# Kernel tuning notes

Measured on AMD Instinct MI355X. Metric: run time of the kernel, lower is better.

The kernel has to match this reference:

```python
import jax, jax.numpy as jnp
import numpy as np

EMB = 1024
H = 16
D = EMB // H  # 64
EPS = 1e-5
SM_SCALE = 1.0  # forward default sm_scale=1.0
CAUSAL = True
NEG = -1e30


def _layernorm(t, g, b):
    # LayerNorm over last dim (head_dim), per torch nn.LayerNorm(head_dim)
    m = jnp.mean(t, axis=-1, keepdims=True)
    v = jnp.mean(jnp.square(t - m), axis=-1, keepdims=True)
    return (t - m) * jax.lax.rsqrt(v + EPS) * g + b


def setup_inputs() -> dict:
    key = jax.random.key(0)
    ks = jax.random.split(key, 8)
    N, L = 2, 2048
    x = jax.random.normal(ks[0], (N, L, EMB), dtype=jnp.float32)
    mask = jnp.ones((N, L), dtype=jnp.int32)  # accepted but unused, as in the torch module
    s = 0.02
    Wq = jax.random.normal(ks[1], (EMB, EMB), dtype=jnp.float32) * s
    Wk = jax.random.normal(ks[2], (EMB, EMB), dtype=jnp.float32) * s
    Wv = jax.random.normal(ks[3], (EMB, EMB), dtype=jnp.float32) * s
    Wo = jax.random.normal(ks[4], (EMB, EMB), dtype=jnp.float32) * s
    bo = jnp.zeros((EMB,), dtype=jnp.float32)
    gq = jnp.ones((D,), dtype=jnp.float32)
    bq = jnp.zeros((D,), dtype=jnp.float32)
    gk = jnp.ones((D,), dtype=jnp.float32)
    bk = jnp.zeros((D,), dtype=jnp.float32)
    return {"x": x, "mask": mask, "Wq": Wq, "Wk": Wk, "Wv": Wv,
            "gq": gq, "bq": bq, "gk": gk, "bk": bk, "Wo": Wo, "bo": bo}


def reference(x, mask, Wq, Wk, Wv, gq, bq, gk, bk, Wo, bo):
    N, L, _ = x.shape
    # QKV projections (torch Linear: x @ W.T), split into heads -> [N, H, L, D]
    q = (x @ Wq.T).reshape(N, L, H, D).transpose(0, 2, 1, 3)
    k = (x @ Wk.T).reshape(N, L, H, D).transpose(0, 2, 1, 3)
    v = (x @ Wv.T).reshape(N, L, H, D).transpose(0, 2, 1, 3)
    # fused_q_norm variant: per-head LayerNorm on Q and K (fused into attention kernel)
    q = _layernorm(q, gq, bq)
    k = _layernorm(k, gk, bk)
    scores = jnp.einsum('nhld,nhmd->nhlm', q, k) * SM_SCALE  # [N,H,L,L]
    if CAUSAL:
        causal = jnp.tril(jnp.ones((L, L), dtype=bool))
        scores = jnp.where(causal, scores, NEG)
    attn = jax.nn.softmax(scores, axis=-1)
    out = jnp.einsum('nhlm,nhmd->nhld', attn, v)
    out = out.transpose(0, 2, 1, 3).reshape(N, L, EMB)
    return out @ Wo.T + bo
```

## Files before the change

### kernel.cpp

```cpp
#include <hip/hip_runtime.h>
#include <stdint.h>

typedef unsigned short u16;
typedef u16   u16x4    __attribute__((ext_vector_type(4)));
typedef u16   u16x8    __attribute__((ext_vector_type(8)));
typedef u16x8 u16x8_ma __attribute__((may_alias));
typedef __bf16 bf16x8  __attribute__((ext_vector_type(8)));
typedef float f32x4    __attribute__((ext_vector_type(4)));
typedef f32x4 f32x4_ma __attribute__((may_alias));

#define EMB    1024
#define NHEAD  16
#define HD     64
#define SEQ    2048
#define NBATCH 2
#define ROWS   (NBATCH*SEQ)
#define SATT   72
#define TSTRIDE 132

__device__ __forceinline__ u16 f2b(float f) {
  uint32_t u; __builtin_memcpy(&u, &f, 4);
  u = u + 0x7fffu + ((u >> 16) & 1u);
  return (u16)(u >> 16);
}
__device__ __forceinline__ u16x8 ld8(const u16* p) { return *(const u16x8_ma*)p; }
__device__ __forceinline__ void  st8(u16* p, u16x8 v) { *(u16x8_ma*)p = v; }
__device__ __forceinline__ bf16x8 asbf(u16x8 v) {
  union { u16x8 u; bf16x8 b; } c; c.u = v; return c.b;
}
__device__ __forceinline__ uint32_t cvtpk(float a, float b) {
  uint32_t r;
  asm("v_cvt_pk_bf16_f32 %0, %1, %2" : "=v"(r) : "v"(a), "v"(b));
  return r;
}
__device__ __forceinline__ void pl32swap(uint32_t &a, uint32_t &b) {
  asm("v_permlane32_swap_b32 %0, %1" : "+v"(a), "+v"(b));
}
__device__ __forceinline__ void pl16swap(uint32_t &a, uint32_t &b) {
  asm("v_permlane16_swap_b32 %0, %1" : "+v"(a), "+v"(b));
}
__device__ __forceinline__ void async_cp16(const u16* g, u16* l) {
  __builtin_amdgcn_global_load_lds(
      (const __attribute__((address_space(1))) void*)g,
      (__attribute__((address_space(3))) void*)l, 16, 0, 0);
}
__device__ __forceinline__ void xcd_swz(int gx, int gy, int &bx, int &by) {
  int lin = bx + gx * by;
  int q = (gx * gy) >> 3;
  int w = (lin & 7) * q + (lin >> 3);
  bx = w % gx; by = w / gx;
}

__global__ __launch_bounds__(256) void cvt_all(
    const float* __restrict__ x,
    const float* __restrict__ w0, const float* __restrict__ w1,
    const float* __restrict__ w2, const float* __restrict__ w3,
    u16* __restrict__ xd, u16* __restrict__ d0, u16* __restrict__ d1,
    u16* __restrict__ d2, u16* __restrict__ d3)
{
  int bid = blockIdx.x;
  const float* s; u16* d; int off;
  if (bid < 4096) { s = x; d = xd; off = bid; }
  else {
    int t = bid - 4096; int m = t >> 10; off = t & 1023;
    switch (m) {
      case 0: s = w0; d = d0; break;
      case 1: s = w1; d = d1; break;
      case 2: s = w2; d = d2; break;
      default: s = w3; d = d3; break;
    }
  }
  size_t i = ((size_t)off * 256 + threadIdx.x) * 4;
  f32x4 v = *(const f32x4_ma*)(s + i);
  u16x4 o;
  #pragma unroll
  for (int j = 0; j < 4; j++) o[j] = f2b(v[j]);
  *(u16x4*)(d + i) = o;
}

template<int AMODE>
__device__ __forceinline__ void gemm_acc_128x128(
    const u16* __restrict__ A, const u16* __restrict__ B,
    int m0, int n0, u16* As, u16* Bs, f32x4 acc[4][4])
{
  const int tid  = threadIdx.x;
  const int lane = tid & 63;
  const int wave = tid >> 6;
  const int wm   = (wave >> 1) * 64;
  const int wn   = (wave & 1) * 64;
  const int ar   = tid >> 2;
  const int ac   = (tid & 3) * 8;
  const int lm   = lane & 15;
  const int lk   = (lane >> 4) * 8;

  #pragma unroll
  for (int i = 0; i < 4; i++)
    #pragma unroll
    for (int j = 0; j < 4; j++)
      #pragma unroll
      for (int e = 0; e < 4; e++) acc[i][j][e] = 0.f;

  for (int k0 = 0; k0 < EMB; k0 += 64) {
    size_t a0[2], a1[2];
    #pragma unroll
    for (int pnl = 0; pnl < 2; pnl++) {
      int kc = k0 + pnl * 32 + ac;
      if (AMODE == 0) {
        a0[pnl] = (size_t)(m0 + ar)      * EMB + kc;
        a1[pnl] = (size_t)(m0 + ar + 64) * EMB + kc;
      } else {
        int h = kc >> 6, d = kc & 63;
        int r0 = m0 + ar, r1 = m0 + ar + 64;
        a0[pnl] = (((size_t)((r0 >> 11) * NHEAD + h)) * SEQ + (r0 & (SEQ-1))) * HD + d;
        a1[pnl] = (((size_t)((r1 >> 11) * NHEAD + h)) * SEQ + (r1 & (SEQ-1))) * HD + d;
      }
    }
    __syncthreads();
    #pragma unroll
    for (int pnl = 0; pnl < 2; pnl++) {
      const int pb = pnl * 4096;
      async_cp16(A + a0[pnl], As + pb + tid * 8);
      async_cp16(A + a1[pnl], As + pb + (tid + 256) * 8);
      async_cp16(B + (size_t)(n0 + ar)      * EMB + k0 + pnl * 32 + ac, Bs + pb + tid * 8);
      async_cp16(B + (size_t)(n0 + ar + 64) * EMB + k0 + pnl * 32 + ac, Bs + pb + (tid + 256) * 8);
    }
    __syncthreads();

    #pragma unroll
    for (int pnl = 0; pnl < 2; pnl++) {
      const int pb = pnl * 4096;
      bf16x8 af[4], bfr[4];
      #pragma unroll
      for (int i = 0; i < 4; i++)
        af[i] = asbf(ld8(As + pb + (wm + i * 16 + lm) * 32 + lk));
      #pragma unroll
      for (int j = 0; j < 4; j++)
        bfr[j] = asbf(ld8(Bs + pb + (wn + j * 16 + lm) * 32 + lk));
      #pragma unroll
      for (int i = 0; i < 4; i++)
        #pragma unroll
        for (int j = 0; j < 4; j++)
          acc[i][j] = __builtin_amdgcn_mfma_f32_16x16x32_bf16(af[i], bfr[j], acc[i][j], 0, 0, 0);
    }
  }
}

__device__ __forceinline__ void epilogue_scatter_ln(
    f32x4 acc[4][4], u16* dst, int m0, int n0, int head_base, int Hdst,
    const float* g, const float* b, int do_ln)
{
  const int lane = threadIdx.x & 63, wave = threadIdx.x >> 6;
  const int wm = (wave >> 1) * 64, wn = (wave & 1) * 64;
  const int lm = lane & 15, quad = lane >> 4;

  float gv[4], bv[4];
  #pragma unroll
  for (int j = 0; j < 4; j++) { gv[j] = g[j * 16 + lm]; bv[j] = b[j * 16 + lm]; }

  #pragma unroll
  for (int i = 0; i < 4; i++)
    #pragma unroll
    for (int r = 0; r < 4; r++) {
      float val[4];
      #pragma unroll
      for (int j = 0; j < 4; j++) val[j] = acc[i][j][r];
      if (do_ln) {
        float s = val[0] + val[1] + val[2] + val[3];
        #pragma unroll
        for (int o = 8; o >= 1; o >>= 1) s += __shfl_xor(s, o, 64);
        float mean = s * (1.f / 64.f);
        float ss = 0.f;
        #pragma unroll
        for (int j = 0; j < 4; j++) { val[j] -= mean; ss += val[j] * val[j]; }
        #pragma unroll
        for (int o = 8; o >= 1; o >>= 1) ss += __shfl_xor(ss, o, 64);
        float inv = rsqrtf(ss * (1.f / 64.f) + 1e-5f);
        #pragma unroll
        for (int j = 0; j < 4; j++) val[j] = val[j] * inv * gv[j] + bv[j];
      }
      int row = m0 + wm + i * 16 + quad * 4 + r;
      int bn = row >> 11, l = row & (SEQ - 1);
      #pragma unroll
      for (int j = 0; j < 4; j++) {
        int col = n0 + wn + j * 16 + lm;
        int hl = (col >> 6) - head_base, d = col & 63;
        dst[(((size_t)(bn * Hdst + hl)) * SEQ + l) * HD + d] = f2b(val[j]);
      }
    }
}

__device__ __forceinline__ void epilogue_transpose_v(
    f32x4 acc[4][4], u16* dst, int m0, int n0, int Hdst, u16* Ts)
{
  const int tid = threadIdx.x, lane = tid & 63, wave = tid >> 6;
  const int wm = (wave >> 1) * 64;
  const int lm = lane & 15, quad = lane >> 4;
  const int bn = m0 >> 11, l0 = m0 & (SEQ - 1);

  #pragma unroll
  for (int pass = 0; pass < 2; ++pass) {
    __syncthreads();
    if ((wave & 1) == pass) {
      #pragma unroll
      for (int i = 0; i < 4; i++)
        #pragma unroll
        for (int j = 0; j < 4; j++)
          #pragma unroll
          for (int r = 0; r < 4; r++)
            Ts[(j * 16 + lm) * TSTRIDE + wm + i * 16 + quad * 4 + r] =
                f2b(acc[i][j][r]);
    }
    __syncthreads();
    const int hl = (n0 >> 6) + pass;
    u16* base = dst + ((size_t)(bn * Hdst + hl)) * HD * SEQ + l0;
    #pragma unroll
    for (int it = 0; it < 4; ++it) {
      int e = it * 2048 + tid * 8;
      int d = e >> 7, l = e & 127;
      st8(base + (size_t)d * SEQ + l, ld8(Ts + d * TSTRIDE + l));
    }
  }
}

__global__ __launch_bounds__(256) void gemm_qk(
    const u16* __restrict__ x,
    const u16* __restrict__ Wq, const u16* __restrict__ Wk,
    const float* __restrict__ gq, const float* __restrict__ bq,
    const float* __restrict__ gk, const float* __restrict__ bk,
    u16* __restrict__ qd, u16* __restrict__ kb)
{
  __shared__ __align__(16) u16 As[128 * 64];
  __shared__ __align__(16) u16 Bs[128 * 64];
  int bx = blockIdx.x, by = blockIdx.y;
  xcd_swz(8, 32, bx, by);
  const int m0 = by * 128, n0 = bx * 128;
  f32x4 acc[4][4];
  if (blockIdx.z == 0) {
    gemm_acc_128x128<0>(x, Wq, m0, n0, As, Bs, acc);
    epilogue_scatter_ln(acc, qd, m0, n0, 0, NHEAD, gq, bq, 1);
  } else {
    gemm_acc_128x128<0>(x, Wk, m0, n0, As, Bs, acc);
    epilogue_scatter_ln(acc, kb, m0, n0, 0, NHEAD, gk, bk, 1);
  }
}

__global__ __launch_bounds__(256) void gemm_v(
    const u16* __restrict__ x, const u16* __restrict__ Wv,
    u16* __restrict__ vb)
{
  __shared__ __align__(16) u16 buf[128 * 64 * 2];
  u16* As = buf;
  u16* Bs = buf + 128 * 64;
  int bx = blockIdx.x, by = blockIdx.y;
  xcd_swz(8, 32, bx, by);
  const int m0 = by * 128, n0 = bx * 128;
  f32x4 acc[4][4];
  gemm_acc_128x128<0>(x, Wv, m0, n0, As, Bs, acc);
  epilogue_transpose_v(acc, vb, m0, n0, NHEAD, buf);
}

__global__ __launch_bounds__(256) void gemm_q(
    const u16* __restrict__ x, const u16* __restrict__ Wq,
    const float* __restrict__ gq, const float* __restrict__ bq,
    u16* __restrict__ qd)
{
  __shared__ __align__(16) u16 As[128 * 64];
  __shared__ __align__(16) u16 Bs[128 * 64];
  int bx = blockIdx.x, by = blockIdx.y;
  xcd_swz(8, 32, bx, by);
  const int m0 = by * 128, n0 = bx * 128;
  f32x4 acc[4][4];
  gemm_acc_128x128<0>(x, Wq, m0, n0, As, Bs, acc);
  epilogue_scatter_ln(acc, qd, m0, n0, 0, NHEAD, gq, bq, 1);
}
__global__ __launch_bounds__(256) void gemm_kv(
    const u16* __restrict__ x,
    const u16* __restrict__ Wk, const u16* __restrict__ Wv,
    const float* __restrict__ gk, const float* __restrict__ bk,
    u16* __restrict__ k, u16* __restrict__ v, int head_lo, int hpp)
{
  __shared__ __align__(16) u16 buf[128 * 64 * 2];
  u16* As = buf;
  u16* Bs = buf + 128 * 64;
  int bx = blockIdx.x, by = blockIdx.y;
  xcd_swz(hpp / 2, 32, bx, by);
  const int m0 = by * 128, n0 = bx * 128;
  const u16* W = (blockIdx.z == 0 ? Wk : Wv) + (size_t)head_lo * HD * EMB;
  f32x4 acc[4][4];
  gemm_acc_128x128<0>(x, W, m0, n0, As, Bs, acc);
  if (blockIdx.z == 0)
    epilogue_scatter_ln(acc, k, m0, n0, 0, hpp, gk, bk, 1);
  else
    epilogue_transpose_v(acc, v, m0, n0, hpp, buf);
}

__global__ __launch_bounds__(256, 4) void attn(
    u16* qd, const u16* __restrict__ K, const u16* __restrict__ V,
    int head_lo, int hpp)
{
  __shared__ __align__(16) u16 Ks[2][64 * SATT];
  __shared__ __align__(16) u16 Vt[2][64 * SATT];

  int p, hl, n;
  if (hpp == NHEAD) {
    const int lin = blockIdx.x + 32 * (blockIdx.y + NHEAD * blockIdx.z);
    const int xcd = lin & 7, idx = lin >> 3;
    const int slot = idx & 3, pp = idx >> 2;
    const int hi = pp >> 3, lo = pp & 7;
    p = (hi & 1) ? (hi * 8 + 7 - lo) : (hi * 8 + lo);
    const int head = xcd * 4 + slot;
    n = head >> 4; hl = head & 15;
  } else {
    hl = blockIdx.y; n = blockIdx.z;
    const int perm = (7 * blockIdx.x + (hl & 7) + 8 * n) & 31;
    p = perm ^ (31 * (hl >> 3));
  }
  const int tid = threadIdx.x, lane = tid & 63, wave = tid >> 6;
  const int lm = lane & 15, quad = lane >> 4, lk = quad * 8;
  u16* Qh = qd + ((size_t)(n * NHEAD + head_lo + hl)) * SEQ * HD;
  const u16* Kh = K + ((size_t)(n * hpp + hl)) * SEQ * HD;
  const u16* Vh = V + ((size_t)(n * hpp + hl)) * HD * SEQ;

  const int sr = tid >> 3;
  const int sc = (tid & 7) * 8;
  const int vd = tid >> 2;
  const int vc = (tid & 3) * 16;

  bf16x8 aq[2];
  #pragma unroll
  for (int ks = 0; ks < 2; ++ks)
    aq[ks] = asbf(ld8(Qh + (size_t)(p * 64 + wave * 16 + lm) * HD + ks * 32 + lk));

  u16x8 kr0, kr1, vr0, vr1;
  kr0 = ld8(Kh + (size_t)(sr)      * HD + sc);
  kr1 = ld8(Kh + (size_t)(sr + 32) * HD + sc);
  vr0 = ld8(Vh + (size_t)vd * SEQ + vc);
  vr1 = ld8(Vh + (size_t)vd * SEQ + vc + 8);
  st8(&Ks[0][sr * SATT + sc], kr0);
  st8(&Ks[0][(sr + 32) * SATT + sc], kr1);
  st8(&Vt[0][vd * SATT + vc], vr0);
  st8(&Vt[0][vd * SATT + vc + 8], vr1);
  kr0 = ld8(Kh + (size_t)(64 + sr)      * HD + sc);
  kr1 = ld8(Kh + (size_t)(64 + sr + 32) * HD + sc);
  vr0 = ld8(Vh + (size_t)vd * SEQ + 64 + vc);
  vr1 = ld8(Vh + (size_t)vd * SEQ + 64 + vc + 8);
  __syncthreads();

  f32x4 oacc[4];
  #pragma unroll
  for (int j = 0; j < 4; j++)
    #pragma unroll
    for (int e = 0; e < 4; e++) oacc[j][e] = 0.f;
  float m_i = -1e30f, psum = 0.f;

  const int qrow = p * 64 + wave * 16 + lm;

  for (int t = 0; t <= p; ++t) {
    const int cur = t & 1;
    if (t < p) {
      const int nb = 1 - cur;
      st8(&Ks[nb][sr * SATT + sc], kr0);
      st8(&Ks[nb][(sr + 32) * SATT + sc], kr1);
      st8(&Vt[nb][vd * SATT + vc], vr0);
      st8(&Vt[nb][vd * SATT + vc + 8], vr1);
      if (t + 1 < p) {
        const size_t base = (size_t)(t + 2) * 64;
        kr0 = ld8(Kh + (base + sr)      * HD + sc);
        kr1 = ld8(Kh + (base + sr + 32) * HD + sc);
        vr0 = ld8(Vh + (size_t)vd * SEQ + base + vc);
        vr1 = ld8(Vh + (size_t)vd * SEQ + base + vc + 8);
      }
    }

    f32x4 s[4];
    #pragma unroll
    for (int j = 0; j < 4; j++)
      #pragma unroll
      for (int e = 0; e < 4; e++) s[j][e] = 0.f;
    __builtin_amdgcn_s_setprio(1);
    #pragma unroll
    for (int ks = 0; ks < 2; ++ks)
      #pragma unroll
      for (int j = 0; j < 4; j++) {
        bf16x8 ak = asbf(ld8(&Ks[cur][(j * 16 + lm) * SATT + ks * 32 + lk]));
        s[j] = __builtin_amdgcn_mfma_f32_16x16x32_bf16(ak, aq[ks], s[j], 0, 0, 0);
      }
    __builtin_amdgcn_s_setprio(0);

    if (t == p) {
      #pragma unroll
      for (int j = 0; j < 4; j++)
        #pragma unroll
        for (int r = 0; r < 4; r++)
          if (t * 64 + j * 16 + quad * 4 + r > qrow) s[j][r] = -1e30f;
    }

    float mx = fmaxf(fmaxf(s[0][0], s[0][1]), fmaxf(s[0][2], s[0][3]));
    #pragma unroll
    for (int j = 1; j < 4; j++)
      mx = fmaxf(mx, fmaxf(fmaxf(s[j][0], s[j][1]), fmaxf(s[j][2], s[j][3])));
    mx = fmaxf(mx, __shfl_xor(mx, 16, 64));
    mx = fmaxf(mx, __shfl_xor(mx, 32, 64));

    const bool defer = __all(mx <= m_i + 8.f);
    float alpha = 1.f;
    if (!defer) {
      const float mnew = fmaxf(m_i, mx);
      alpha = __expf(m_i - mnew);
      m_i = mnew;
    }
    float part = 0.f;
    #pragma unroll
    for (int j = 0; j < 4; j++)
      #pragma unroll
      for (int r = 0; r < 4; r++) {
        float pv = __expf(s[j][r] - m_i);
        s[j][r] = pv;
        part += pv;
      }
    if (defer) {
      psum += part;
    } else {
      psum = psum * alpha + part;
      float ar_[4];
      #pragma unroll
      for (int r = 0; r < 4; r++)
        ar_[r] = __shfl(alpha, (lane & 48) | (quad * 4 + r), 64);
      #pragma unroll
      for (int j = 0; j < 4; j++)
        #pragma unroll
        for (int r = 0; r < 4; r++) oacc[j][r] *= ar_[r];
    }

    uint32_t u[8];
    #pragma unroll
    for (int j = 0; j < 4; j++) {
      u[2 * j]     = cvtpk(s[j][0], s[j][1]);
      u[2 * j + 1] = cvtpk(s[j][2], s[j][3]);
    }

    __builtin_amdgcn_s_setprio(1);
    #pragma unroll
    for (int ks = 0; ks < 2; ++ks) {
      uint32_t a0 = u[ks * 4 + 0], a1 = u[ks * 4 + 1];
      uint32_t a2 = u[ks * 4 + 2], a3 = u[ks * 4 + 3];
      pl32swap(a0, a2);
      pl16swap(a0, a2);
      pl32swap(a1, a3);
      pl16swap(a1, a3);
      union { uint32_t w[4]; bf16x8 v; } cv;
      cv.w[0] = a0; cv.w[1] = a1; cv.w[2] = a2; cv.w[3] = a3;
      bf16x8 ap = cv.v;
      #pragma unroll
      for (int j = 0; j < 4; j++) {
        bf16x8 bv = asbf(ld8(&Vt[cur][(j * 16 + lm) * SATT + ks * 32 + lk]));
        oacc[j] = __builtin_amdgcn_mfma_f32_16x16x32_bf16(ap, bv, oacc[j], 0, 0, 0);
      }
    }
    __builtin_amdgcn_s_setprio(0);
    __syncthreads();
  }

  float s_ = psum;
  s_ += __shfl_xor(s_, 16, 64);
  s_ += __shfl_xor(s_, 32, 64);
  const float inv = 1.0f / s_;
  float ir_[4];
  #pragma unroll
  for (int r = 0; r < 4; r++)
    ir_[r] = __shfl(inv, (lane & 48) | (quad * 4 + r), 64);
  #pragma unroll
  for (int r = 0; r < 4; r++) {
    const int row = p * 64 + wave * 16 + quad * 4 + r;
    #pragma unroll
    for (int j = 0; j < 4; j++)
      Qh[(size_t)row * HD + j * 16 + lm] = f2b(oacc[j][r] * ir_[r]);
  }
}

__global__ __launch_bounds__(256) void gemm_out(
    const u16* __restrict__ ao, const u16* __restrict__ Wo,
    const float* __restrict__ bo, float* __restrict__ out)
{
  __shared__ __align__(16) u16 As[64 * 64];
  __shared__ __align__(16) u16 Bs[128 * 64];
  int bx = blockIdx.x, by = blockIdx.y;
  xcd_swz(8, 64, bx, by);
  const int m0 = by * 64, n0 = bx * 128;
  const int tid  = threadIdx.x;
  const int lane = tid & 63;
  const int wave = tid >> 6;
  const int wm   = (wave >> 1) * 32;
  const int wn   = (wave & 1) * 64;
  const int ar   = tid >> 2;
  const int ac   = (tid & 3) * 8;
  const int lm   = lane & 15;
  const int lk   = (lane >> 4) * 8;

  f32x4 acc[2][4];
  #pragma unroll
  for (int i = 0; i < 2; i++)
    #pragma unroll
    for (int j = 0; j < 4; j++)
      #pragma unroll
      for (int e = 0; e < 4; e++) acc[i][j][e] = 0.f;

  for (int k0 = 0; k0 < EMB; k0 += 64) {
    size_t aoff[2];
    #pragma unroll
    for (int pnl = 0; pnl < 2; pnl++) {
      int kc = k0 + pnl * 32 + ac, h = kc >> 6, d = kc & 63;
      int r0 = m0 + ar;
      aoff[pnl] = (((size_t)((r0 >> 11) * NHEAD + h)) * SEQ + (r0 & (SEQ-1))) * HD + d;
    }
    __syncthreads();
    #pragma unroll
    for (int pnl = 0; pnl < 2; pnl++) {
      async_cp16(ao + aoff[pnl], As + pnl * 2048 + tid * 8);
      async_cp16(Wo + (size_t)(n0 + ar)      * EMB + k0 + pnl * 32 + ac, Bs + pnl * 4096 + tid * 8);
      async_cp16(Wo + (size_t)(n0 + ar + 64) * EMB + k0 + pnl * 32 + ac, Bs + pnl * 4096 + (tid + 256) * 8);
    }
    __syncthreads();

    #pragma unroll
    for (int pnl = 0; pnl < 2; pnl++) {
      bf16x8 af[2], bfr[4];
      #pragma unroll
      for (int i = 0; i < 2; i++)
        af[i] = asbf(ld8(As + pnl * 2048 + (wm + i * 16 + lm) * 32 + lk));
      #pragma unroll
      for (int j = 0; j < 4; j++)
        bfr[j] = asbf(ld8(Bs + pnl * 4096 + (wn + j * 16 + lm) * 32 + lk));
      #pragma unroll
      for (int i = 0; i < 2; i++)
        #pragma unroll
        for (int j = 0; j < 4; j++)
          acc[i][j] = __builtin_amdgcn_mfma_f32_16x16x32_bf16(af[i], bfr[j], acc[i][j], 0, 0, 0);
    }
  }

  const int quad = lane >> 4;
  #pragma unroll
  for (int j = 0; j < 4; j++) {
    int col = n0 + wn + j * 16 + lm;
    float bias = bo[col];
    #pragma unroll
    for (int i = 0; i < 2; i++)
      #pragma unroll
      for (int r = 0; r < 4; r++) {
        int row = m0 + wm + i * 16 + quad * 4 + r;
        out[(size_t)row * EMB + col] = acc[i][j][r] + bias;
      }
  }
}

extern "C" void kernel_launch(void* const* d_in, const int* in_sizes, int n_in,
                              void* d_out, int out_size, void* d_ws, size_t ws_size,
                              hipStream_t stream)
{
  const float* xf  = (const float*)d_in[0];
  const float* Wqf = (const float*)d_in[2];
  const float* Wkf = (const float*)d_in[3];
  const float* Wvf = (const float*)d_in[4];
  const float* gq  = (const float*)d_in[5];
  const float* bq  = (const float*)d_in[6];
  const float* gk  = (const float*)d_in[7];
  const float* bk  = (const float*)d_in[8];
  const float* Wof = (const float*)d_in[9];
  const float* bo  = (const float*)d_in[10];

  const size_t MB = 1u << 20;
  u16* xb  = (u16*)d_ws;
  u16* wqb = xb  + (size_t)ROWS * EMB;
  u16* wkb = wqb + (size_t)EMB * EMB;
  u16* wvb = wkb + (size_t)EMB * EMB;
  u16* wob = wvb + (size_t)EMB * EMB;
  u16* kvbase = wob + (size_t)EMB * EMB;

  size_t avail = (ws_size > 16 * MB) ? ws_size - 16 * MB : 2 * MB;
  int hpp = NHEAD;
  while ((size_t)hpp * MB > avail && hpp > 2) hpp >>= 1;
  const size_t kv_elems = (size_t)hpp * NBATCH * SEQ * HD;
  u16* kbuf = kvbase;
  u16* vbuf = kbuf + kv_elems;

  u16* qd = (u16*)d_in[0];
  float* out = (float*)d_out;

  cvt_all<<<dim3(8192), 256, 0, stream>>>(xf, Wqf, Wkf, Wvf, Wof,
                                          xb, wqb, wkb, wvb, wob);
  if (hpp == NHEAD) {
    gemm_qk<<<dim3(8, 32, 2), 256, 0, stream>>>(xb, wqb, wkb,
                                                gq, bq, gk, bk, qd, kbuf);
    gemm_v<<<dim3(8, 32), 256, 0, stream>>>(xb, wvb, vbuf);
    attn<<<dim3(32, NHEAD, NBATCH), 256, 0, stream>>>(qd, kbuf, vbuf, 0, NHEAD);
  } else {
    gemm_q<<<dim3(8, 32), 256, 0, stream>>>(xb, wqb, gq, bq, qd);
    for (int g = 0; g < NHEAD / hpp; ++g) {
      gemm_kv<<<dim3(hpp / 2, 32, 2), 256, 0, stream>>>(xb, wkb, wvb, gk, bk,
                                                        kbuf, vbuf, g * hpp, hpp);
      attn<<<dim3(32, hpp, NBATCH), 256, 0, stream>>>(qd, kbuf, vbuf, g * hpp, hpp);
    }
  }
  gemm_out<<<dim3(8, 64), 256, 0, stream>>>(qd, wob, bo, out);
}
```

Baseline: 198.9 us.

## Stage attention K/V tiles via async global-to-LDS copies with XOR-swizzled layout

Replaces the register-staged K/V prefetch in the attention kernel (global load into registers, then LDS store) with direct asynchronous 16-byte global-to-LDS copies issued one tile ahead. Because each lane now writes a contiguous 16-byte chunk, the padded SATT=72 row stride becomes an unpadded 64-wide layout with an XOR swizzle on the column group, applied to both the copy sources and the MFMA operand reads, to avoid bank conflicts. This removes the VGPRs and store instructions used for staging and may raise overlap. The risk is that completion of the async copies has to be covered by the existing barriers; if async_cp16 does not wait on its own loads, the kernel could read stale tiles.

Measured after the change: 200.3 us. Within noise of the previous version (+0.7%).

```diff
diff --git a/kernel.cpp b/kernel.cpp
--- a/kernel.cpp
+++ b/kernel.cpp
@@ -15,7 +15,6 @@
 #define SEQ    2048
 #define NBATCH 2
 #define ROWS   (NBATCH*SEQ)
-#define SATT   72
 #define TSTRIDE 132
 
 __device__ __forceinline__ u16 f2b(float f) {
@@ -298,8 +297,8 @@
     u16* qd, const u16* __restrict__ K, const u16* __restrict__ V,
     int head_lo, int hpp)
 {
-  __shared__ __align__(16) u16 Ks[2][64 * SATT];
-  __shared__ __align__(16) u16 Vt[2][64 * SATT];
+  __shared__ __align__(16) u16 Ks[2][64 * 64];
+  __shared__ __align__(16) u16 Vt[2][64 * 64];
 
   int p, hl, n;
   if (hpp == NHEAD) {
@@ -316,34 +315,34 @@
     p = perm ^ (31 * (hl >> 3));
   }
   const int tid = threadIdx.x, lane = tid & 63, wave = tid >> 6;
-  const int lm = lane & 15, quad = lane >> 4, lk = quad * 8;
+  const int lm = lane & 15, quad = lane >> 4;
   u16* Qh = qd + ((size_t)(n * NHEAD + head_lo + hl)) * SEQ * HD;
   const u16* Kh = K + ((size_t)(n * hpp + hl)) * SEQ * HD;
   const u16* Vh = V + ((size_t)(n * hpp + hl)) * HD * SEQ;
 
-  const int sr = tid >> 3;
-  const int sc = (tid & 7) * 8;
-  const int vd = tid >> 2;
-  const int vc = (tid & 3) * 16;
-
+  const int c0 = tid, c1 = tid + 256;
+  const int kk0 = c0 >> 3, kd0 = ((c0 & 7) ^ (kk0 & 7)) * 8;
+  const int kk1 = c1 >> 3, kd1 = ((c1 & 7) ^ (kk1 & 7)) * 8;
+  const int vd0 = kk0, vg0 = kd0;
+  const int vd1 = kk1, vg1 = kd1;
+
+  const int lk = quad * 8;
   bf16x8 aq[2];
   #pragma unroll
   for (int ks = 0; ks < 2; ++ks)
     aq[ks] = asbf(ld8(Qh + (size_t)(p * 64 + wave * 16 + lm) * HD + ks * 32 + lk));
 
-  u16x8 kr0, kr1, vr0, vr1;
-  kr0 = ld8(Kh + (size_t)(sr)      * HD + sc);
-  kr1 = ld8(Kh + (size_t)(sr + 32) * HD + sc);
-  vr0 = ld8(Vh + (size_t)vd * SEQ + vc);
-  vr1 = ld8(Vh + (size_t)vd * SEQ + vc + 8);
-  st8(&Ks[0][sr * SATT + sc], kr0);
-  st8(&Ks[0][(sr + 32) * SATT + sc], kr1);
-  st8(&Vt[0][vd * SATT + vc], vr0);
-  st8(&Vt[0][vd * SATT + vc + 8], vr1);
-  kr0 = ld8(Kh + (size_t)(64 + sr)      * HD + sc);
-  kr1 = ld8(Kh + (size_t)(64 + sr + 32) * HD + sc);
-  vr0 = ld8(Vh + (size_t)vd * SEQ + 64 + vc);
-  vr1 = ld8(Vh + (size_t)vd * SEQ + 64 + vc + 8);
+  #define STAGE(buf, t)                                                        \
+    {                                                                          \
+      const u16* Kt = Kh + (size_t)(t) * 64 * HD;                              \
+      const u16* Vg = Vh + (size_t)(t) * 64;                                   \
+      async_cp16(Kt + (size_t)kk0 * HD + kd0, &Ks[buf][0] + tid * 8);          \
+      async_cp16(Kt + (size_t)kk1 * HD + kd1, &Ks[buf][0] + (tid + 256) * 8);  \
+      async_cp16(Vg + (size_t)vd0 * SEQ + vg0, &Vt[buf][0] + tid * 8);         \
+      async_cp16(Vg + (size_t)vd1 * SEQ + vg1, &Vt[buf][0] + (tid + 256) * 8); \
+    }
+
+  STAGE(0, 0);
   __syncthreads();
 
   f32x4 oacc[4];
@@ -354,23 +353,11 @@
   float m_i = -1e30f, psum = 0.f;
 
   const int qrow = p * 64 + wave * 16 + lm;
+  const int xh = lm & 7;
 
   for (int t = 0; t <= p; ++t) {
     const int cur = t & 1;
-    if (t < p) {
-      const int nb = 1 - cur;
-      st8(&Ks[nb][sr * SATT + sc], kr0);
-      st8(&Ks[nb][(sr + 32) * SATT + sc], kr1);
-      st8(&Vt[nb][vd * SATT + vc], vr0);
-      st8(&Vt[nb][vd * SATT + vc + 8], vr1);
-      if (t + 1 < p) {
-        const size_t base = (size_t)(t + 2) * 64;
-        kr0 = ld8(Kh + (base + sr)      * HD + sc);
-        kr1 = ld8(Kh + (base + sr + 32) * HD + sc);
-        vr0 = ld8(Vh + (size_t)vd * SEQ + base + vc);
-        vr1 = ld8(Vh + (size_t)vd * SEQ + base + vc + 8);
-      }
-    }
+    if (t < p) STAGE(1 - cur, t + 1);
 
     f32x4 s[4];
     #pragma unroll
@@ -382,7 +369,8 @@
     for (int ks = 0; ks < 2; ++ks)
       #pragma unroll
       for (int j = 0; j < 4; j++) {
-        bf16x8 ak = asbf(ld8(&Ks[cur][(j * 16 + lm) * SATT + ks * 32 + lk]));
+        bf16x8 ak = asbf(ld8(&Ks[cur][((j * 16 + lm) << 6) +
+                                      (((ks * 4 + quad) ^ xh) << 3)]));
         s[j] = __builtin_amdgcn_mfma_f32_16x16x32_bf16(ak, aq[ks], s[j], 0, 0, 0);
       }
     __builtin_amdgcn_s_setprio(0);
@@ -453,13 +441,15 @@
       bf16x8 ap = cv.v;
       #pragma unroll
       for (int j = 0; j < 4; j++) {
-        bf16x8 bv = asbf(ld8(&Vt[cur][(j * 16 + lm) * SATT + ks * 32 + lk]));
+        bf16x8 bv = asbf(ld8(&Vt[cur][((j * 16 + lm) << 6) +
+                                      (((ks * 4 + quad) ^ xh) << 3)]));
         oacc[j] = __builtin_amdgcn_mfma_f32_16x16x32_bf16(ap, bv, oacc[j], 0, 0, 0);
       }
     }
     __builtin_amdgcn_s_setprio(0);
     __syncthreads();
   }
+  #undef STAGE
 
   float s_ = psum;
   s_ += __shfl_xor(s_, 16, 64);
```
